# Optimization experiments

Hardware: AMD Instinct MI355X
Metric: run time of the kernel (lower is better)

## Reference

```python
import jax, jax.numpy as jnp
import numpy as np


def setup_inputs() -> dict:
    key = jax.random.key(0)
    k1, k2 = jax.random.split(key)
    N, C, D = 16384, 4096, 1024
    x = jax.random.normal(k1, (N, D), dtype=jnp.float32)
    # torch.rand -> uniform [0, 1)
    prototype = jax.random.uniform(k2, (C, D), dtype=jnp.float32)
    return {"x": x, "prototype": prototype}


def reference(x, prototype):
    # Pairwise squared Euclidean distance:
    #   d[n, c] = sum_k (x[n, k] - p[c, k])^2
    # GEMM-based decomposition avoids the O(N*C*D) broadcast intermediate.
    x_sq = jnp.sum(x * x, axis=-1, keepdims=True)            # [N, 1]
    p_sq = jnp.sum(prototype * prototype, axis=-1)            # [C]
    cross = jnp.einsum('nd,cd->nc', x, prototype)             # [N, C] GEMM
    d = x_sq + p_sq[None, :] - 2.0 * cross                    # [N, C]
    return d
```

## Files before the change

### kernel.cpp

```cpp
#include <hip/hip_runtime.h>
#include <hip/hip_bf16.h>
#include <stdint.h>

#define NX 16384
#define NC 4096
#define DIM 1024

typedef __attribute__((ext_vector_type(8))) short bf16x8;
typedef __attribute__((ext_vector_type(4))) float f32x4;


__device__ inline unsigned short f2bf_rn(float f) {
  union { float f; unsigned u; } v; v.f = f;
  unsigned u = v.u;
  unsigned r = (u + 0x7FFFu + ((u >> 16) & 1u)) >> 16;
  return (unsigned short)r;
}

__device__ inline void gload_lds16(const void* g, void* l) {
  __builtin_amdgcn_global_load_lds(
      (const __attribute__((address_space(1))) void*)g,
      (__attribute__((address_space(3))) void*)l,
      16, 0, 0);
}

__device__ inline f32x4 mfma_bf16_16x16x32(bf16x8 a, bf16x8 b, f32x4 c) {
  asm("v_mfma_f32_16x16x32_bf16 %0, %1, %2, %0" : "+v"(c) : "v"(a), "v"(b));
  return c;
}


__global__ __launch_bounds__(256) void convert_all(
    const float* __restrict__ x, const float* __restrict__ p,
    unsigned short* __restrict__ xb, unsigned short* __restrict__ pb,
    float* __restrict__ xsq, float* __restrict__ psq) {
  const int gw = blockIdx.x * 4 + (threadIdx.x >> 6);
  const int lane = threadIdx.x & 63;
  const float* src; unsigned short* dst; float* sq; int row;
  if (gw < NX) { src = x; dst = xb; sq = xsq; row = gw; }
  else         { src = p; dst = pb; sq = psq; row = gw - NX; }
  const size_t base = (size_t)row * DIM;

  float s = 0.f;
  #pragma unroll
  for (int j = 0; j < 4; ++j) {
    const float4 v = *(const float4*)(src + base + j * 256 + lane * 4);
    s += v.x * v.x + v.y * v.y + v.z * v.z + v.w * v.w;
    ushort4 o;
    o.x = f2bf_rn(v.x); o.y = f2bf_rn(v.y);
    o.z = f2bf_rn(v.z); o.w = f2bf_rn(v.w);
    *(ushort4*)(dst + base + j * 256 + lane * 4) = o;
  }
  #pragma unroll
  for (int off = 32; off; off >>= 1) s += __shfl_xor(s, off, 64);
  if (lane == 0) sq[row] = s;
}


#define BM 256
#define BN 256
#define BK 64
#define NT (DIM / BK)

__global__ __launch_bounds__(512, 2) void dist_gemm(
    const unsigned short* __restrict__ xb,
    const unsigned short* __restrict__ pb,
    const float* __restrict__ xsq,
    const float* __restrict__ psq,
    float* __restrict__ out) {
  extern __shared__ char lds[];

  const int tid  = threadIdx.x;
  const int wid  = tid >> 6;
  const int lane = tid & 63;
  const int wm = wid >> 2;
  const int wn = wid & 3;

  const int bid = blockIdx.x;
  const int xcd = bid & 7;
  const int idx = bid >> 3;
  const int g   = idx >> 4;
  const int l4  = idx & 15;
  const int tm  = xcd * 8 + (g & 1) * 4 + (l4 >> 2);
  const int tn  = (g >> 1) * 4 + (l4 & 3);
  const int row0 = tm * BM, col0 = tn * BN;

  const int srow = wid * 8 + (lane >> 3);
  const int scb  = ((lane & 7) ^ (lane >> 3)) << 4;
  const char* gA = (const char*)xb + (size_t)(row0 + srow) * (DIM * 2) + scb;
  const char* gB = (const char*)pb + (size_t)(col0 + srow) * (DIM * 2) + scb;

  const int sx   = (lane & 7) << 4;
  const int hi16 = (lane >> 4) << 4;
  const int arow = (wm * 128 + (lane & 15)) * 128;
  const int brow = (wn * 64  + (lane & 15)) * 128;
  const int csw0 = (hi16 + 0)  ^ sx;
  const int csw1 = (hi16 + 64) ^ sx;

  f32x4 acc[8][4] = {};

#define STAGE(kt, bufsel) do {                                               \
    char* lA_ = lds + (bufsel) * 65536;                                      \
    char* lB_ = lA_ + 32768;                                                 \
    _Pragma("unroll")                                                        \
    for (int it = 0; it < 4; ++it) {                                         \
      gload_lds16(gA + (size_t)(kt) * 128 + (size_t)it * 64 * (DIM * 2),     \
                  lA_ + it * 8192 + wid * 1024);                             \
      gload_lds16(gB + (size_t)(kt) * 128 + (size_t)it * 64 * (DIM * 2),     \
                  lB_ + it * 8192 + wid * 1024);                             \
    }                                                                        \
  } while (0)

#define COMPUTE(bufsel) do {                                                 \
    const char* lA_ = lds + (bufsel) * 65536;                                \
    const char* lB_ = lA_ + 32768;                                           \
    bf16x8 a[8], b[4];                                                       \
    _Pragma("unroll")                                                        \
    for (int m = 0; m < 8; ++m)                                              \
      a[m] = *(const bf16x8*)(lA_ + arow + m * 2048 + csw0);                 \
    _Pragma("unroll")                                                        \
    for (int n = 0; n < 4; ++n)                                              \
      b[n] = *(const bf16x8*)(lB_ + brow + n * 2048 + csw0);                 \
    __builtin_amdgcn_s_setprio(1);                                           \
    _Pragma("unroll")                                                        \
    for (int m = 0; m < 8; ++m)                                              \
      _Pragma("unroll")                                                      \
      for (int n = 0; n < 4; ++n)                                            \
        acc[m][n] = mfma_bf16_16x16x32(a[m], b[n], acc[m][n]);               \
    __builtin_amdgcn_s_setprio(0);                                           \
    _Pragma("unroll")                                                        \
    for (int m = 0; m < 8; ++m)                                              \
      a[m] = *(const bf16x8*)(lA_ + arow + m * 2048 + csw1);                 \
    _Pragma("unroll")                                                        \
    for (int n = 0; n < 4; ++n)                                              \
      b[n] = *(const bf16x8*)(lB_ + brow + n * 2048 + csw1);                 \
    __builtin_amdgcn_s_setprio(1);                                           \
    _Pragma("unroll")                                                        \
    for (int m = 0; m < 8; ++m)                                              \
      _Pragma("unroll")                                                      \
      for (int n = 0; n < 4; ++n)                                            \
        acc[m][n] = mfma_bf16_16x16x32(a[m], b[n], acc[m][n]);               \
    __builtin_amdgcn_s_setprio(0);                                           \
  } while (0)

  STAGE(0, 0);

  #pragma unroll 2
  for (int t = 0; t < NT - 1; ++t) {
    STAGE(t + 1, (t + 1) & 1);
    asm volatile("s_waitcnt vmcnt(8)" ::: "memory");
    __builtin_amdgcn_s_barrier();
    asm volatile("" ::: "memory");
    COMPUTE(t & 1);
    asm volatile("" ::: "memory");
    __builtin_amdgcn_s_barrier();
  }
  asm volatile("s_waitcnt vmcnt(0)" ::: "memory");
  __builtin_amdgcn_s_barrier();
  asm volatile("" ::: "memory");
  COMPUTE((NT - 1) & 1);

#undef STAGE
#undef COMPUTE

  const int orow = row0 + wm * 128 + ((lane >> 4) << 2);
  const int ocol = col0 + wn * 64 + (lane & 15);
  float pv[4];
  #pragma unroll
  for (int n = 0; n < 4; ++n) pv[n] = psq[ocol + n * 16];

  #pragma unroll
  for (int m = 0; m < 8; ++m) {
    #pragma unroll
    for (int ri = 0; ri < 4; ++ri) {
      const int r = orow + m * 16 + ri;
      const float xv = xsq[r];
      #pragma unroll
      for (int n = 0; n < 4; ++n)
        out[(size_t)r * NC + ocol + n * 16] = xv + pv[n] - 2.0f * acc[m][n][ri];
    }
  }
}


extern "C" void kernel_launch(void* const* d_in, const int* in_sizes, int n_in,
                              void* d_out, int out_size, void* d_ws, size_t ws_size,
                              hipStream_t stream) {
  const float* x = (const float*)d_in[0];
  const float* p = (const float*)d_in[1];
  float* out = (float*)d_out;

  char* ws = (char*)d_ws;
  unsigned short* xb  = (unsigned short*)ws;
  unsigned short* pbb = (unsigned short*)(ws + (size_t)NX * DIM * 2);
  float* xsq = (float*)(ws + (size_t)NX * DIM * 2 + (size_t)NC * DIM * 2);
  float* psq = xsq + NX;

  convert_all<<<(NX + NC) / 4, 256, 0, stream>>>(x, p, xb, pbb, xsq, psq);

  static int attr_done = 0;
  (void)hipFuncSetAttribute((const void*)dist_gemm,
                            hipFuncAttributeMaxDynamicSharedMemorySize, 131072);
  (void)attr_done;

  dist_gemm<<<dim3((NX / BM) * (NC / BN)), dim3(512), 131072, stream>>>(
      xb, pbb, xsq, psq, out);
}
```

Before: 439.0 us.

## Shrink GEMM tile to 256x128 with triple-buffered LDS and split staging

Changes the distance GEMM tile from 256x256 to 256x128, giving 8 waves arranged 4x2 with 64x64 sub-tiles each. It replaces the double-buffered LDS with a three-buffer ring of 48KB, prefetching two K-steps ahead, and splits each prefetch into two halves issued between the sub-K compute phases. Block-to-tile mapping and the LDS swizzle pattern are also changed. The goal is better overlap of global loads with MFMA work, more blocks for load balance, and fewer registers. The cost is lower arithmetic intensity per block and more barriers per iteration. LDS use grows to 144KB per block, which likely limits each CU to one block despite the launch bound of 2.

```diff
diff --git a/kernel.cpp b/kernel.cpp
--- a/kernel.cpp
+++ b/kernel.cpp
@@ -58,9 +58,10 @@
 
 
 #define BM 256
-#define BN 256
+#define BN 128
 #define BK 64
 #define NT (DIM / BK)
+#define LBUF 49152
 
 __global__ __launch_bounds__(512, 2) void dist_gemm(
     const unsigned short* __restrict__ xb,
@@ -73,104 +74,113 @@
   const int tid  = threadIdx.x;
   const int wid  = tid >> 6;
   const int lane = tid & 63;
-  const int wm = wid >> 2;
-  const int wn = wid & 3;
+  const int wm = wid >> 1;
+  const int wn = wid & 1;
 
   const int bid = blockIdx.x;
   const int xcd = bid & 7;
   const int idx = bid >> 3;
-  const int g   = idx >> 4;
-  const int l4  = idx & 15;
-  const int tm  = xcd * 8 + (g & 1) * 4 + (l4 >> 2);
-  const int tn  = (g >> 1) * 4 + (l4 & 3);
+  const int tm  = xcd * 8 + (idx >> 5);
+  const int tn  = idx & 31;
   const int row0 = tm * BM, col0 = tn * BN;
 
   const int srow = wid * 8 + (lane >> 3);
-  const int scb  = ((lane & 7) ^ (lane >> 3)) << 4;
+  const int scb  = (((lane & 7) ^ (((lane >> 5) & 1) << 1)) << 4);
   const char* gA = (const char*)xb + (size_t)(row0 + srow) * (DIM * 2) + scb;
   const char* gB = (const char*)pb + (size_t)(col0 + srow) * (DIM * 2) + scb;
 
-  const int sx   = (lane & 7) << 4;
-  const int hi16 = (lane >> 4) << 4;
-  const int arow = (wm * 128 + (lane & 15)) * 128;
-  const int brow = (wn * 64  + (lane & 15)) * 128;
-  const int csw0 = (hi16 + 0)  ^ sx;
-  const int csw1 = (hi16 + 64) ^ sx;
-
-  f32x4 acc[8][4] = {};
-
-#define STAGE(kt, bufsel) do {                                               \
-    char* lA_ = lds + (bufsel) * 65536;                                      \
-    char* lB_ = lA_ + 32768;                                                 \
-    _Pragma("unroll")                                                        \
-    for (int it = 0; it < 4; ++it) {                                         \
-      gload_lds16(gA + (size_t)(kt) * 128 + (size_t)it * 64 * (DIM * 2),     \
-                  lA_ + it * 8192 + wid * 1024);                             \
-      gload_lds16(gB + (size_t)(kt) * 128 + (size_t)it * 64 * (DIM * 2),     \
-                  lB_ + it * 8192 + wid * 1024);                             \
-    }                                                                        \
+  const int fr  = lane & 15;
+  const int rsw = (lane & 4) << 3;
+  const int g16 = (lane >> 4) << 4;
+  const int aro = (wm * 64 + fr) * 128;
+  const int bro = (wn * 64 + fr) * 128 + 32768;
+  const int c0  = g16 ^ rsw;
+  const int c1  = 64 + (g16 ^ rsw);
+
+  f32x4 acc[4][4] = {};
+
+  char* p0 = lds;
+  char* p1 = lds + LBUF;
+  char* p2 = lds + 2 * LBUF;
+
+#define STAGE_A012(kt, dst) do {                                        \
+    const size_t ko = (size_t)(kt) * 128;                               \
+    gload_lds16(gA + ko,          (dst) + wid * 1024);                  \
+    gload_lds16(gA + ko + 131072, (dst) + 8192  + wid * 1024);          \
+    gload_lds16(gA + ko + 262144, (dst) + 16384 + wid * 1024);          \
   } while (0)
-
-#define COMPUTE(bufsel) do {                                                 \
-    const char* lA_ = lds + (bufsel) * 65536;                                \
-    const char* lB_ = lA_ + 32768;                                           \
-    bf16x8 a[8], b[4];                                                       \
-    _Pragma("unroll")                                                        \
-    for (int m = 0; m < 8; ++m)                                              \
-      a[m] = *(const bf16x8*)(lA_ + arow + m * 2048 + csw0);                 \
-    _Pragma("unroll")                                                        \
-    for (int n = 0; n < 4; ++n)                                              \
-      b[n] = *(const bf16x8*)(lB_ + brow + n * 2048 + csw0);                 \
-    __builtin_amdgcn_s_setprio(1);                                           \
-    _Pragma("unroll")                                                        \
-    for (int m = 0; m < 8; ++m)                                              \
-      _Pragma("unroll")                                                      \
-      for (int n = 0; n < 4; ++n)                                            \
-        acc[m][n] = mfma_bf16_16x16x32(a[m], b[n], acc[m][n]);               \
-    __builtin_amdgcn_s_setprio(0);                                           \
-    _Pragma("unroll")                                                        \
-    for (int m = 0; m < 8; ++m)                                              \
-      a[m] = *(const bf16x8*)(lA_ + arow + m * 2048 + csw1);                 \
-    _Pragma("unroll")                                                        \
-    for (int n = 0; n < 4; ++n)                                              \
-      b[n] = *(const bf16x8*)(lB_ + brow + n * 2048 + csw1);                 \
-    __builtin_amdgcn_s_setprio(1);                                           \
-    _Pragma("unroll")                                                        \
-    for (int m = 0; m < 8; ++m)                                              \
-      _Pragma("unroll")                                                      \
-      for (int n = 0; n < 4; ++n)                                            \
-        acc[m][n] = mfma_bf16_16x16x32(a[m], b[n], acc[m][n]);               \
-    __builtin_amdgcn_s_setprio(0);                                           \
+#define STAGE_A3B01(kt, dst) do {                                       \
+    const size_t ko = (size_t)(kt) * 128;                               \
+    gload_lds16(gA + ko + 393216, (dst) + 24576 + wid * 1024);          \
+    gload_lds16(gB + ko,          (dst) + 32768 + wid * 1024);          \
+    gload_lds16(gB + ko + 131072, (dst) + 40960 + wid * 1024);          \
   } while (0)
 
-  STAGE(0, 0);
-
-  #pragma unroll 2
-  for (int t = 0; t < NT - 1; ++t) {
-    STAGE(t + 1, (t + 1) & 1);
-    asm volatile("s_waitcnt vmcnt(8)" ::: "memory");
-    __builtin_amdgcn_s_barrier();
-    asm volatile("" ::: "memory");
-    COMPUTE(t & 1);
-    asm volatile("" ::: "memory");
-    __builtin_amdgcn_s_barrier();
-  }
-  asm volatile("s_waitcnt vmcnt(0)" ::: "memory");
+  STAGE_A012(0, p0); STAGE_A3B01(0, p0);
+  STAGE_A012(1, p1); STAGE_A3B01(1, p1);
+  asm volatile("s_waitcnt vmcnt(6)" ::: "memory");
   __builtin_amdgcn_s_barrier();
   asm volatile("" ::: "memory");
-  COMPUTE((NT - 1) & 1);
-
-#undef STAGE
-#undef COMPUTE
-
-  const int orow = row0 + wm * 128 + ((lane >> 4) << 2);
-  const int ocol = col0 + wn * 64 + (lane & 15);
+
+  for (int t = 0; t < NT; ++t) {
+    const bool more = (t < NT - 2);
+
+    bf16x8 a0[4], b0[4];
+    #pragma unroll
+    for (int m = 0; m < 4; ++m) a0[m] = *(const bf16x8*)(p0 + aro + m * 2048 + c0);
+    #pragma unroll
+    for (int n = 0; n < 4; ++n) b0[n] = *(const bf16x8*)(p0 + bro + n * 2048 + c0);
+    if (more) STAGE_A012(t + 2, p2);
+    asm volatile("" ::: "memory");
+    __builtin_amdgcn_s_barrier();
+    asm volatile("" ::: "memory");
+    __builtin_amdgcn_s_setprio(1);
+    #pragma unroll
+    for (int m = 0; m < 4; ++m)
+      #pragma unroll
+      for (int n = 0; n < 4; ++n)
+        acc[m][n] = mfma_bf16_16x16x32(a0[m], b0[n], acc[m][n]);
+    __builtin_amdgcn_s_setprio(0);
+    asm volatile("" ::: "memory");
+    __builtin_amdgcn_s_barrier();
+    asm volatile("" ::: "memory");
+
+    bf16x8 a1[4], b1[4];
+    #pragma unroll
+    for (int m = 0; m < 4; ++m) a1[m] = *(const bf16x8*)(p0 + aro + m * 2048 + c1);
+    #pragma unroll
+    for (int n = 0; n < 4; ++n) b1[n] = *(const bf16x8*)(p0 + bro + n * 2048 + c1);
+    if (more) STAGE_A3B01(t + 2, p2);
+    asm volatile("" ::: "memory");
+    __builtin_amdgcn_s_barrier();
+    asm volatile("" ::: "memory");
+    __builtin_amdgcn_s_setprio(1);
+    #pragma unroll
+    for (int m = 0; m < 4; ++m)
+      #pragma unroll
+      for (int n = 0; n < 4; ++n)
+        acc[m][n] = mfma_bf16_16x16x32(a1[m], b1[n], acc[m][n]);
+    __builtin_amdgcn_s_setprio(0);
+    if (more)            asm volatile("s_waitcnt vmcnt(6)" ::: "memory");
+    else if (t == NT - 2) asm volatile("s_waitcnt vmcnt(0)" ::: "memory");
+    asm volatile("" ::: "memory");
+    __builtin_amdgcn_s_barrier();
+    asm volatile("" ::: "memory");
+
+    char* tmp = p0; p0 = p1; p1 = p2; p2 = tmp;
+  }
+
+#undef STAGE_A012
+#undef STAGE_A3B01
+
+  const int orow = row0 + wm * 64 + ((lane >> 4) << 2);
+  const int ocol = col0 + wn * 64 + fr;
   float pv[4];
   #pragma unroll
   for (int n = 0; n < 4; ++n) pv[n] = psq[ocol + n * 16];
 
   #pragma unroll
-  for (int m = 0; m < 8; ++m) {
+  for (int m = 0; m < 4; ++m) {
     #pragma unroll
     for (int ri = 0; ri < 4; ++ri) {
       const int r = orow + m * 16 + ri;
@@ -198,11 +208,10 @@
 
   convert_all<<<(NX + NC) / 4, 256, 0, stream>>>(x, p, xb, pbb, xsq, psq);
 
-  static int attr_done = 0;
   (void)hipFuncSetAttribute((const void*)dist_gemm,
-                            hipFuncAttributeMaxDynamicSharedMemorySize, 131072);
-  (void)attr_done;
-
-  dist_gemm<<<dim3((NX / BM) * (NC / BN)), dim3(512), 131072, stream>>>(
-      xb, pbb, xsq, psq, out);
-}
+                            hipFuncAttributeMaxDynamicSharedMemorySize,
+                            3 * LBUF);
+
+  dim3 grid((NX / BM) * (NC / BN));
+  dist_gemm<<<grid, dim3(512), 3 * LBUF, stream>>>(xb, pbb, xsq, psq, out);
+}
```

New measurement: 466.5 us. 6.3% more time.
